# Performance work log

Measured on AMD Instinct MI355X. Metric: run time of the kernel, lower is better.

The kernel has to match this reference:

```python
import jax, jax.numpy as jnp
import numpy as np

NEG_BIG = -9e15
ALPHA = 0.2  # LeakyReLU negative slope
B, N, F_IN, F_OUT = 8, 2048, 128, 128


def setup_inputs() -> dict:
    key = jax.random.key(0)
    k1, k2, k3, k4 = jax.random.split(key, 4)
    inp = jax.random.normal(k1, (B, N, F_IN), dtype=jnp.float32)
    adj = jax.random.randint(k2, (B, N, N), 0, 2, dtype=jnp.int32)
    W = 0.02 * jax.random.normal(k3, (F_OUT, F_IN), dtype=jnp.float32)  # nn.Linear weight [out,in]
    a = 0.02 * jax.random.normal(k4, (1, 2 * F_OUT), dtype=jnp.float32)  # attention vector [1, 2F]
    return {"input": inp, "adj": adj, "W": W, "a": a}


def reference(input, adj, W, a):
    # h = input @ W^T : [B, N, F_OUT]
    h = jnp.einsum("bnf,of->bno", input, W)
    f_out = h.shape[-1]
    # Decompose a . [h_i || h_j] = (h_i . a1) + (h_j . a2) -- same math as the
    # explicit repeat_interleave/repeat/cat, without the O(N^2 * 2F) tensor.
    a1 = a[0, :f_out]
    a2 = a[0, f_out:]
    s1 = h @ a1  # [B, N] score for source node i
    s2 = h @ a2  # [B, N] score for target node j
    e = jax.nn.leaky_relu(s1[:, :, None] + s2[:, None, :], negative_slope=ALPHA)  # [B,N,N]
    masked = jnp.where(adj > 0, e, NEG_BIG)
    attention = jax.nn.softmax(masked, axis=-1)
    # dropout p=0.0 (eval) -> identity
    h_prime = jnp.einsum("bnm,bmo->bno", attention, h)
    return h_prime
```

## Files before the change

### kernel.cpp

```cpp
#include <hip/hip_runtime.h>
#include <stdint.h>


#define B_ 8
#define N_ 2048
#define FD 128
#define ALPHA_ 0.2f
#define TJ 64
#define NCHL 16
#define CHUNK_U4 1024

typedef __attribute__((ext_vector_type(8))) short short8;
typedef __attribute__((ext_vector_type(4))) float f32x4;

#define HCHUNK(o, jc) ((((o) * 16) + ((jc) ^ ((o) & 15))) * 8)
#define HC64(o, jc) ((o) * 8 + ((jc) ^ ((o) & 7)))

__device__ __forceinline__ float bf2f(unsigned short u) {
    union { uint32_t i; float f; } v; v.i = ((uint32_t)u) << 16; return v.f;
}
__device__ __forceinline__ unsigned short f2bf(float f) {
    union { float f; uint32_t i; } v; v.f = f;
    uint32_t x = v.i;
    uint32_t r = (x + 0x7fffu + ((x >> 16) & 1u)) >> 16;
    return (unsigned short)r;
}

__device__ __forceinline__ void gl2lds16(const uint4* g, uint4* l) {
    __builtin_amdgcn_global_load_lds(
        (const __attribute__((address_space(1))) uint32_t*)g,
        (__attribute__((address_space(3))) uint32_t*)l, 16, 0, 0);
}

__global__ __launch_bounds__(256) void gat_h(
    const float* __restrict__ x,
    const float* __restrict__ W,
    const float* __restrict__ a,
    unsigned short* __restrict__ hT,
    float* __restrict__ s1o, float* __restrict__ s2o)
{
    __shared__ __align__(16) unsigned short Wlds[FD * FD];

    const int bid = blockIdx.x;
    const int tid = threadIdx.x;
    const int w = tid >> 6;
    const int lane = tid & 63;
    const int m = lane & 15;
    const int quad = lane >> 4;
    const int arow = bid * 64 + w * 16 + m;

#pragma unroll
    for (int it = 0; it < 8; it++) {
        int cid = it * 256 + tid;
        int o = cid >> 4, kc = cid & 15;
        const float* wp = W + (size_t)o * FD + kc * 8;
        float4 w0 = *(const float4*)wp;
        float4 w1 = *(const float4*)(wp + 4);
        uint4 pk;
        pk.x = (uint32_t)f2bf(w0.x) | ((uint32_t)f2bf(w0.y) << 16);
        pk.y = (uint32_t)f2bf(w0.z) | ((uint32_t)f2bf(w0.w) << 16);
        pk.z = (uint32_t)f2bf(w1.x) | ((uint32_t)f2bf(w1.y) << 16);
        pk.w = (uint32_t)f2bf(w1.z) | ((uint32_t)f2bf(w1.w) << 16);
        *(uint4*)&Wlds[HCHUNK(o, kc)] = pk;
    }
    __syncthreads();

    f32x4 acc[8];
#pragma unroll
    for (int ot = 0; ot < 8; ot++) acc[ot] = (f32x4){0.f, 0.f, 0.f, 0.f};

#pragma unroll
    for (int ks = 0; ks < 4; ks++) {
        const float* xp = x + (size_t)arow * FD + ks * 32 + quad * 8;
        float4 x0 = *(const float4*)xp;
        float4 x1 = *(const float4*)(xp + 4);
        float xv[8] = {x0.x, x0.y, x0.z, x0.w, x1.x, x1.y, x1.z, x1.w};
        union { unsigned short us[8]; short8 v; } ahi, alo;
#pragma unroll
        for (int jj = 0; jj < 8; jj++) {
            unsigned short hi = f2bf(xv[jj]);
            ahi.us[jj] = hi;
            alo.us[jj] = f2bf(xv[jj] - bf2f(hi));
        }
#pragma unroll
        for (int ot = 0; ot < 8; ot++) {
            union { uint4 u; short8 v; } bw;
            bw.u = *(const uint4*)&Wlds[HCHUNK(ot * 16 + m, ks * 4 + quad)];
            acc[ot] = __builtin_amdgcn_mfma_f32_16x16x32_bf16(ahi.v, bw.v, acc[ot], 0, 0, 0);
            acc[ot] = __builtin_amdgcn_mfma_f32_16x16x32_bf16(alo.v, bw.v, acc[ot], 0, 0, 0);
        }
    }

    const int rc0 = bid * 64 + w * 16 + quad * 4;
    const int bb = rc0 >> 11;
    const int jb = rc0 & (N_ - 1);
    const int kc = jb >> 6;
    const int jcl = (jb & 63) >> 3;
    const int off = jb & 7;
    unsigned short* hTb = hT + (size_t)bb * FD * N_ + (size_t)kc * (CHUNK_U4 * 8);
    float s1p[4] = {0.f, 0.f, 0.f, 0.f};
    float s2p[4] = {0.f, 0.f, 0.f, 0.f};
#pragma unroll
    for (int ot = 0; ot < 8; ot++) {
        const int o = ot * 16 + m;
        uint2 pk;
        pk.x = (uint32_t)f2bf(acc[ot][0]) | ((uint32_t)f2bf(acc[ot][1]) << 16);
        pk.y = (uint32_t)f2bf(acc[ot][2]) | ((uint32_t)f2bf(acc[ot][3]) << 16);
        *(uint2*)(hTb + (size_t)HC64(o, jcl) * 8 + off) = pk;
        float a1v = a[o], a2v = a[FD + o];
#pragma unroll
        for (int r = 0; r < 4; r++) {
            s1p[r] += acc[ot][r] * a1v;
            s2p[r] += acc[ot][r] * a2v;
        }
    }
#pragma unroll
    for (int offx = 8; offx >= 1; offx >>= 1) {
#pragma unroll
        for (int r = 0; r < 4; r++) {
            s1p[r] += __shfl_xor(s1p[r], offx);
            s2p[r] += __shfl_xor(s2p[r], offx);
        }
    }
    if (m == 0) {
#pragma unroll
        for (int r = 0; r < 4; r++) {
            s1o[rc0 + r] = s1p[r];
            s2o[rc0 + r] = s2p[r];
        }
    }
}

__global__ __launch_bounds__(256, 2) void gat_attn(
    const int* __restrict__ adj,
    const unsigned short* __restrict__ hT,
    const float* __restrict__ s1,
    const float* __restrict__ s2,
    float* __restrict__ out)
{
    __shared__ __align__(16) uint4 hbuf[2][2][CHUNK_U4];

    const int bid = blockIdx.x;
    const int b = bid >> 6;
    const int i0 = (bid & 63) * 32;
    const int tid = threadIdx.x;
    const int lane = tid & 63;
    const int w = tid >> 6;
    const int jh = w >> 1;
    const int rh = w & 1;
    const int m = lane & 15;
    const int quad = lane >> 4;

    const int irow = i0 + rh * 16 + m;
    const float s1v = s1[b * N_ + irow];
    const int* adjrow = adj + ((size_t)(b * N_ + irow)) * N_ + jh * 1024;
    const uint4* hTc = (const uint4*)(hT + (size_t)b * FD * N_)
                       + (size_t)jh * NCHL * CHUNK_U4;
    const float* s2b = s2 + b * N_ + jh * 1024;

#pragma unroll
    for (int it = 0; it < 8; it++)
        gl2lds16(&hTc[it * 128 + rh * 64 + lane], &hbuf[jh][0][it * 128 + rh * 64]);
    int4 acur[4];
    float4 scur[4];
#pragma unroll
    for (int ks = 0; ks < 2; ks++) {
        acur[2 * ks]     = *(const int4*)(adjrow + ks * 32 + quad * 8);
        acur[2 * ks + 1] = *(const int4*)(adjrow + ks * 32 + quad * 8 + 4);
        scur[2 * ks]     = *(const float4*)(s2b + ks * 32 + quad * 8);
        scur[2 * ks + 1] = *(const float4*)(s2b + ks * 32 + quad * 8 + 4);
    }
    __syncthreads();

    f32x4 acc[8];
#pragma unroll
    for (int ot = 0; ot < 8; ot++) acc[ot] = (f32x4){0.f, 0.f, 0.f, 0.f};
    float rs_loc = 0.f;

    for (int k = 0; k < NCHL; k++) {
        const int buf = k & 1;
        const bool more = (k + 1 < NCHL);
        int4 anext[4];
        float4 snext[4];
        if (more) {
#pragma unroll
            for (int it = 0; it < 8; it++)
                gl2lds16(&hTc[(size_t)(k + 1) * CHUNK_U4 + it * 128 + rh * 64 + lane],
                         &hbuf[jh][buf ^ 1][it * 128 + rh * 64]);
            const int j1 = (k + 1) * TJ;
#pragma unroll
            for (int ks = 0; ks < 2; ks++) {
                anext[2 * ks]     = *(const int4*)(adjrow + j1 + ks * 32 + quad * 8);
                anext[2 * ks + 1] = *(const int4*)(adjrow + j1 + ks * 32 + quad * 8 + 4);
                snext[2 * ks]     = *(const float4*)(s2b + j1 + ks * 32 + quad * 8);
                snext[2 * ks + 1] = *(const float4*)(s2b + j1 + ks * 32 + quad * 8 + 4);
            }
        }

#pragma unroll
        for (int ks = 0; ks < 2; ks++) {
            float4 sa = scur[2 * ks], sb = scur[2 * ks + 1];
            float sarr[8] = {sa.x, sa.y, sa.z, sa.w, sb.x, sb.y, sb.z, sb.w};
            int4 A0 = acur[2 * ks], A1 = acur[2 * ks + 1];
            int aarr[8] = {A0.x, A0.y, A0.z, A0.w, A1.x, A1.y, A1.z, A1.w};
            union { unsigned short us[8]; short8 v; } af;
#pragma unroll
            for (int jj = 0; jj < 8; jj++) {
                float e = s1v + sarr[jj];
                e = (e > 0.f) ? e : (ALPHA_ * e);
                float p = (aarr[jj] > 0) ? __expf(e) : 0.f;
                rs_loc += p;
                af.us[jj] = f2bf(p);
            }
            const int jc = ks * 4 + quad;
#pragma unroll
            for (int ot = 0; ot < 8; ot++) {
                const int o = ot * 16 + m;
                union { uint4 u; short8 v; } bf;
                bf.u = *(const uint4*)&hbuf[jh][buf][HC64(o, jc)];
                acc[ot] = __builtin_amdgcn_mfma_f32_16x16x32_bf16(af.v, bf.v, acc[ot], 0, 0, 0);
            }
        }

        __syncthreads();
        if (more) {
#pragma unroll
            for (int q = 0; q < 4; q++) { acur[q] = anext[q]; scur[q] = snext[q]; }
        }
    }

    float* xch = (float*)&hbuf[0][0][0];
    rs_loc += __shfl_xor(rs_loc, 16);
    rs_loc += __shfl_xor(rs_loc, 32);
    if (jh == 1) {
#pragma unroll
        for (int ot = 0; ot < 8; ot++)
#pragma unroll
            for (int r = 0; r < 4; r++)
                xch[rh * 2048 + (quad * 4 + r) * 128 + ot * 16 + m] = acc[ot][r];
        if (quad == 0) xch[4096 + rh * 16 + m] = rs_loc;
    }
    __syncthreads();
    if (jh == 0) {
        float rinv[4];
#pragma unroll
        for (int r = 0; r < 4; r++) {
            const int p = quad * 4 + r;
            rinv[r] = 1.0f / (__shfl(rs_loc, p) + xch[4096 + rh * 16 + p]);
        }
        float* outp = out + (size_t)(b * N_ + i0 + rh * 16) * FD;
#pragma unroll
        for (int ot = 0; ot < 8; ot++) {
            const int col = ot * 16 + m;
#pragma unroll
            for (int r = 0; r < 4; r++) {
                float v = acc[ot][r] + xch[rh * 2048 + (quad * 4 + r) * 128 + col];
                outp[(size_t)(quad * 4 + r) * FD + col] = v * rinv[r];
            }
        }
    }
}

extern "C" void kernel_launch(void* const* d_in, const int* in_sizes, int n_in,
                              void* d_out, int out_size, void* d_ws, size_t ws_size,
                              hipStream_t stream) {
    const void* xv = d_in[0];
    const void* adjv = d_in[1];
    const void* Wv = d_in[2];
    const void* av = d_in[3];
    for (int i = 0; i < n_in; i++) {
        switch (in_sizes[i]) {
            case 2097152:  xv = d_in[i]; break;
            case 33554432: adjv = d_in[i]; break;
            case 16384:    Wv = d_in[i]; break;
            case 256:      av = d_in[i]; break;
            default: break;
        }
    }
    const float* x = (const float*)xv;
    const int* adj = (const int*)adjv;
    const float* W = (const float*)Wv;
    const float* a = (const float*)av;
    float* out = (float*)d_out;

    char* p = (char*)d_ws;
    unsigned short* hT = (unsigned short*)p;  p += (size_t)B_ * FD * N_ * 2;
    float* s1 = (float*)p;                    p += (size_t)B_ * N_ * 4;
    float* s2 = (float*)p;

    gat_h<<<256, 256, 0, stream>>>(x, W, a, hT, s1, s2);
    gat_attn<<<512, 256, 0, stream>>>(adj, hT, s1, s2, out);
}
```

Baseline: 215.4 us.

## Read h directly from global memory, split j across four waves per 16-row block

The attention kernel no longer stages hT chunks in LDS with global_load_lds double buffering. Each wave now loads B fragments straight from a plain transposed hT layout in global memory, and each block handles 16 rows with four waves splitting the j range. Partial results are reduced through a small LDS buffer. This removes the per-chunk barriers and the swizzled staging, and raises occupancy with more blocks. In exchange, each wave reads h from L2/global without LDS reuse, which can expose memory latency.

```diff
diff --git a/kernel.cpp b/kernel.cpp
--- a/kernel.cpp
+++ b/kernel.cpp
@@ -6,15 +6,11 @@
 #define N_ 2048
 #define FD 128
 #define ALPHA_ 0.2f
-#define TJ 64
-#define NCHL 16
-#define CHUNK_U4 1024
 
 typedef __attribute__((ext_vector_type(8))) short short8;
 typedef __attribute__((ext_vector_type(4))) float f32x4;
 
 #define HCHUNK(o, jc) ((((o) * 16) + ((jc) ^ ((o) & 15))) * 8)
-#define HC64(o, jc) ((o) * 8 + ((jc) ^ ((o) & 7)))
 
 __device__ __forceinline__ float bf2f(unsigned short u) {
     union { uint32_t i; float f; } v; v.i = ((uint32_t)u) << 16; return v.f;
@@ -24,12 +20,6 @@
     uint32_t x = v.i;
     uint32_t r = (x + 0x7fffu + ((x >> 16) & 1u)) >> 16;
     return (unsigned short)r;
-}
-
-__device__ __forceinline__ void gl2lds16(const uint4* g, uint4* l) {
-    __builtin_amdgcn_global_load_lds(
-        (const __attribute__((address_space(1))) uint32_t*)g,
-        (__attribute__((address_space(3))) uint32_t*)l, 16, 0, 0);
 }
 
 __global__ __launch_bounds__(256) void gat_h(
@@ -94,10 +84,7 @@
     const int rc0 = bid * 64 + w * 16 + quad * 4;
     const int bb = rc0 >> 11;
     const int jb = rc0 & (N_ - 1);
-    const int kc = jb >> 6;
-    const int jcl = (jb & 63) >> 3;
-    const int off = jb & 7;
-    unsigned short* hTb = hT + (size_t)bb * FD * N_ + (size_t)kc * (CHUNK_U4 * 8);
+    unsigned short* hTb = hT + (size_t)bb * FD * N_ + jb;
     float s1p[4] = {0.f, 0.f, 0.f, 0.f};
     float s2p[4] = {0.f, 0.f, 0.f, 0.f};
 #pragma unroll
@@ -106,7 +93,7 @@
         uint2 pk;
         pk.x = (uint32_t)f2bf(acc[ot][0]) | ((uint32_t)f2bf(acc[ot][1]) << 16);
         pk.y = (uint32_t)f2bf(acc[ot][2]) | ((uint32_t)f2bf(acc[ot][3]) << 16);
-        *(uint2*)(hTb + (size_t)HC64(o, jcl) * 8 + off) = pk;
+        *(uint2*)(hTb + (size_t)o * N_) = pk;
         float a1v = a[o], a2v = a[FD + o];
 #pragma unroll
         for (int r = 0; r < 4; r++) {
@@ -131,75 +118,64 @@
     }
 }
 
-__global__ __launch_bounds__(256, 2) void gat_attn(
+__global__ __launch_bounds__(256, 4) void gat_attn(
     const int* __restrict__ adj,
     const unsigned short* __restrict__ hT,
     const float* __restrict__ s1,
     const float* __restrict__ s2,
     float* __restrict__ out)
 {
-    __shared__ __align__(16) uint4 hbuf[2][2][CHUNK_U4];
+    __shared__ float xch[4][16][130];
+    __shared__ float rsl[4][16];
 
     const int bid = blockIdx.x;
-    const int b = bid >> 6;
-    const int i0 = (bid & 63) * 32;
+    const int b = bid & 7;
+    const int ib = bid >> 3;
+    const int i0 = ib * 16;
     const int tid = threadIdx.x;
     const int lane = tid & 63;
     const int w = tid >> 6;
-    const int jh = w >> 1;
-    const int rh = w & 1;
     const int m = lane & 15;
     const int quad = lane >> 4;
 
-    const int irow = i0 + rh * 16 + m;
+    const int irow = i0 + m;
     const float s1v = s1[b * N_ + irow];
-    const int* adjrow = adj + ((size_t)(b * N_ + irow)) * N_ + jh * 1024;
-    const uint4* hTc = (const uint4*)(hT + (size_t)b * FD * N_)
-                       + (size_t)jh * NCHL * CHUNK_U4;
-    const float* s2b = s2 + b * N_ + jh * 1024;
-
-#pragma unroll
-    for (int it = 0; it < 8; it++)
-        gl2lds16(&hTc[it * 128 + rh * 64 + lane], &hbuf[jh][0][it * 128 + rh * 64]);
-    int4 acur[4];
-    float4 scur[4];
+    const int* adjrow = adj + ((size_t)(b * N_ + irow)) * N_ + w * 512;
+    const float* s2b = s2 + b * N_ + w * 512;
+    const unsigned short* hTb = hT + (size_t)b * FD * N_ + (size_t)m * N_ + w * 512;
+
+    f32x4 acc[8];
+#pragma unroll
+    for (int ot = 0; ot < 8; ot++) acc[ot] = (f32x4){0.f, 0.f, 0.f, 0.f};
+    float rs_loc = 0.f;
+
+    int4 acur[4], anext[4];
 #pragma unroll
     for (int ks = 0; ks < 2; ks++) {
         acur[2 * ks]     = *(const int4*)(adjrow + ks * 32 + quad * 8);
         acur[2 * ks + 1] = *(const int4*)(adjrow + ks * 32 + quad * 8 + 4);
-        scur[2 * ks]     = *(const float4*)(s2b + ks * 32 + quad * 8);
-        scur[2 * ks + 1] = *(const float4*)(s2b + ks * 32 + quad * 8 + 4);
-    }
-    __syncthreads();
-
-    f32x4 acc[8];
-#pragma unroll
-    for (int ot = 0; ot < 8; ot++) acc[ot] = (f32x4){0.f, 0.f, 0.f, 0.f};
-    float rs_loc = 0.f;
-
-    for (int k = 0; k < NCHL; k++) {
-        const int buf = k & 1;
-        const bool more = (k + 1 < NCHL);
-        int4 anext[4];
-        float4 snext[4];
-        if (more) {
-#pragma unroll
-            for (int it = 0; it < 8; it++)
-                gl2lds16(&hTc[(size_t)(k + 1) * CHUNK_U4 + it * 128 + rh * 64 + lane],
-                         &hbuf[jh][buf ^ 1][it * 128 + rh * 64]);
-            const int j1 = (k + 1) * TJ;
+    }
+
+#pragma unroll 1
+    for (int k = 0; k < 8; k++) {
+        if (k < 7) {
+            const int j1 = (k + 1) * 64;
 #pragma unroll
             for (int ks = 0; ks < 2; ks++) {
                 anext[2 * ks]     = *(const int4*)(adjrow + j1 + ks * 32 + quad * 8);
                 anext[2 * ks + 1] = *(const int4*)(adjrow + j1 + ks * 32 + quad * 8 + 4);
-                snext[2 * ks]     = *(const float4*)(s2b + j1 + ks * 32 + quad * 8);
-                snext[2 * ks + 1] = *(const float4*)(s2b + j1 + ks * 32 + quad * 8 + 4);
             }
         }
-
+        const int jc0 = k * 64;
 #pragma unroll
         for (int ks = 0; ks < 2; ks++) {
-            float4 sa = scur[2 * ks], sb = scur[2 * ks + 1];
+            uint4 bw[8];
+#pragma unroll
+            for (int ot = 0; ot < 8; ot++)
+                bw[ot] = *(const uint4*)(hTb + (size_t)ot * 16 * N_ + jc0 + ks * 32 + quad * 8);
+
+            const float4 sa = *(const float4*)(s2b + jc0 + ks * 32 + quad * 8);
+            const float4 sb = *(const float4*)(s2b + jc0 + ks * 32 + quad * 8 + 4);
             float sarr[8] = {sa.x, sa.y, sa.z, sa.w, sb.x, sb.y, sb.z, sb.w};
             int4 A0 = acur[2 * ks], A1 = acur[2 * ks + 1];
             int aarr[8] = {A0.x, A0.y, A0.z, A0.w, A1.x, A1.y, A1.z, A1.w};
@@ -212,52 +188,39 @@
                 rs_loc += p;
                 af.us[jj] = f2bf(p);
             }
-            const int jc = ks * 4 + quad;
 #pragma unroll
             for (int ot = 0; ot < 8; ot++) {
-                const int o = ot * 16 + m;
                 union { uint4 u; short8 v; } bf;
-                bf.u = *(const uint4*)&hbuf[jh][buf][HC64(o, jc)];
+                bf.u = bw[ot];
                 acc[ot] = __builtin_amdgcn_mfma_f32_16x16x32_bf16(af.v, bf.v, acc[ot], 0, 0, 0);
             }
         }
-
-        __syncthreads();
-        if (more) {
-#pragma unroll
-            for (int q = 0; q < 4; q++) { acur[q] = anext[q]; scur[q] = snext[q]; }
-        }
-    }
-
-    float* xch = (float*)&hbuf[0][0][0];
+        if (k < 7) {
+#pragma unroll
+            for (int q = 0; q < 4; q++) acur[q] = anext[q];
+        }
+    }
+
     rs_loc += __shfl_xor(rs_loc, 16);
     rs_loc += __shfl_xor(rs_loc, 32);
-    if (jh == 1) {
-#pragma unroll
-        for (int ot = 0; ot < 8; ot++)
-#pragma unroll
-            for (int r = 0; r < 4; r++)
-                xch[rh * 2048 + (quad * 4 + r) * 128 + ot * 16 + m] = acc[ot][r];
-        if (quad == 0) xch[4096 + rh * 16 + m] = rs_loc;
-    }
+
+#pragma unroll
+    for (int ot = 0; ot < 8; ot++)
+#pragma unroll
+        for (int r = 0; r < 4; r++)
+            xch[w][quad * 4 + r][ot * 16 + m] = acc[ot][r];
+    if (quad == 0) rsl[w][m] = rs_loc;
     __syncthreads();
-    if (jh == 0) {
-        float rinv[4];
-#pragma unroll
-        for (int r = 0; r < 4; r++) {
-            const int p = quad * 4 + r;
-            rinv[r] = 1.0f / (__shfl(rs_loc, p) + xch[4096 + rh * 16 + p]);
-        }
-        float* outp = out + (size_t)(b * N_ + i0 + rh * 16) * FD;
-#pragma unroll
-        for (int ot = 0; ot < 8; ot++) {
-            const int col = ot * 16 + m;
-#pragma unroll
-            for (int r = 0; r < 4; r++) {
-                float v = acc[ot][r] + xch[rh * 2048 + (quad * 4 + r) * 128 + col];
-                outp[(size_t)(quad * 4 + r) * FD + col] = v * rinv[r];
-            }
-        }
+
+    const int oo = w * 32 + (lane & 31);
+    const int rbase = (lane >> 5) * 8;
+    float* outb = out + (size_t)(b * N_ + i0) * FD;
+#pragma unroll
+    for (int rr = 0; rr < 8; rr++) {
+        const int row = rbase + rr;
+        float p = xch[0][row][oo] + xch[1][row][oo] + xch[2][row][oo] + xch[3][row][oo];
+        float rt = rsl[0][row] + rsl[1][row] + rsl[2][row] + rsl[3][row];
+        outb[(size_t)row * FD + oo] = p * (1.0f / rt);
     }
 }
 
@@ -289,5 +252,5 @@
     float* s2 = (float*)p;
 
     gat_h<<<256, 256, 0, stream>>>(x, W, a, hT, s1, s2);
-    gat_attn<<<512, 256, 0, stream>>>(adj, hT, s1, s2, out);
-}
+    gat_attn<<<1024, 256, 0, stream>>>(adj, hT, s1, s2, out);
+}
```

Measured after the change: 260.2 us. 20.8% more time.
